# Kernel optimization log

Measured on AMD Instinct MI355X. Metric: run time of the kernel, lower is better.

## Reference

```python
import jax, jax.numpy as jnp
import numpy as np

_GROUP_SIZES = [4096, 2048, 1024, 8192, 512, 3072, 6144, 1024]
_K = 2048
_N = 2048


def setup_inputs() -> dict:
    key = jax.random.key(0)
    keys = jax.random.split(key, len(_GROUP_SIZES) + 1)
    inp = {}
    for i, m in enumerate(_GROUP_SIZES):
        inp[f"A{i}"] = jax.random.normal(keys[i], (m, _K), dtype=jnp.float32)
    inp["B_shared"] = jax.random.normal(keys[-1], (_K, _N), dtype=jnp.float32)
    return inp


def reference(A0, A1, A2, A3, A4, A5, A6, A7, B_shared):
    # torch: cat([a @ B for a in group_A], dim=0)
    # Concatenating ragged groups first and doing one GEMM is the same math
    # (row-block structure of matmul), expressed as a single fused contraction.
    A_cat = jnp.concatenate([A0, A1, A2, A3, A4, A5, A6, A7], axis=0)  # [M_total, K]
    return A_cat @ B_shared  # [M_total, N]
```

## Files before the change

kernel.cpp:

```cpp
#include <hip/hip_runtime.h>
#include <hip/hip_bf16.h>

using short8  = __attribute__((ext_vector_type(8))) short;
using ushort8 = __attribute__((ext_vector_type(8))) unsigned short;
using f32x4   = __attribute__((ext_vector_type(4))) float;

#define GLB(p)  ((const __attribute__((address_space(1))) void*)(p))
#define LDSP(p) ((__attribute__((address_space(3))) void*)(p))

static __device__ __forceinline__ unsigned short f2bf(float f) {
    union { float f; unsigned u; } v; v.f = f;
    unsigned u = v.u;
    u += 0x7fffu + ((u >> 16) & 1u);
    return (unsigned short)(u >> 16);
}

#define K_DIM 2048
#define N_DIM 2048
#define M_TOTAL 26112
#define N_GROUPS 8

__global__ __launch_bounds__(256) void cvt_a_all(
        const float* __restrict__ A0, const float* __restrict__ A1,
        const float* __restrict__ A2, const float* __restrict__ A3,
        const float* __restrict__ A4, const float* __restrict__ A5,
        const float* __restrict__ A6, const float* __restrict__ A7,
        unsigned short* __restrict__ Acat) {
    int b = blockIdx.x;
    const float* src; int gb;
    if      (b < 256)  { src = A0; gb = 0;    }
    else if (b < 384)  { src = A1; gb = 256;  }
    else if (b < 448)  { src = A2; gb = 384;  }
    else if (b < 960)  { src = A3; gb = 448;  }
    else if (b < 992)  { src = A4; gb = 960;  }
    else if (b < 1184) { src = A5; gb = 992;  }
    else if (b < 1568) { src = A6; gb = 1184; }
    else               { src = A7; gb = 1568; }
    const float* s   = src  + (long)(b - gb) * 16 * K_DIM;
    unsigned short* d = Acat + (long)b * 16 * K_DIM;
    int t = threadIdx.x;
#pragma unroll 4
    for (int i = 0; i < 16; ++i) {
        long off = (long)i * K_DIM + t * 8;
        float4 x = *(const float4*)(s + off);
        float4 y = *(const float4*)(s + off + 4);
        ushort8 o;
        o[0] = f2bf(x.x); o[1] = f2bf(x.y); o[2] = f2bf(x.z); o[3] = f2bf(x.w);
        o[4] = f2bf(y.x); o[5] = f2bf(y.y); o[6] = f2bf(y.z); o[7] = f2bf(y.w);
        *(ushort8*)(d + off) = o;
    }
}

__global__ __launch_bounds__(256) void cvt_bt_kernel(const float* __restrict__ B,
                                                     unsigned short* __restrict__ Bt) {
    __shared__ float t[32][33];
    int bx = blockIdx.x, by = blockIdx.y;
    int tx = threadIdx.x, ty = threadIdx.y;
#pragma unroll
    for (int i = 0; i < 32; i += 8)
        t[ty + i][tx] = B[(long)(by * 32 + ty + i) * N_DIM + bx * 32 + tx];
    __syncthreads();
#pragma unroll
    for (int i = 0; i < 32; i += 8)
        Bt[(long)(bx * 32 + ty + i) * K_DIM + by * 32 + tx] = f2bf(t[tx][ty + i]);
}


#define PBAR() __builtin_amdgcn_s_barrier()
#define LGKM0() asm volatile("s_waitcnt lgkmcnt(0)" ::: "memory")
#define VMC(n)  asm volatile("s_waitcnt vmcnt(" #n ")" ::: "memory")

#define ST_A(BUF, H, L, TT)                                                        \
    __builtin_amdgcn_global_load_lds(                                              \
        GLB(aSt + (long)((H) * 128 + (L) * 64) * K_DIM + (TT) * 64),               \
        LDSP(lds + (BUF) * 32768 + (H) * 8192 + (L) * 4096 + w * 512), 16, 0, 0)
#define ST_B(BUF, H, L, TT)                                                        \
    __builtin_amdgcn_global_load_lds(                                              \
        GLB(bSt + (long)((H) * 128 + (L) * 64) * K_DIM + (TT) * 64),               \
        LDSP(lds + (BUF) * 32768 + 16384 + (H) * 8192 + (L) * 4096 + w * 512), 16, 0, 0)

#define MMQ(MH, NH, AV, BV)                                                        \
    _Pragma("unroll") for (int i = 0; i < 4; ++i)                                  \
    _Pragma("unroll") for (int j = 0; j < 2; ++j)                                  \
        acc[(MH) * 4 + i][(NH) * 2 + j] = __builtin_amdgcn_mfma_f32_16x16x32_bf16( \
            AV[i], BV[j], acc[(MH) * 4 + i][(NH) * 2 + j], 0, 0, 0);

#define TILE(BUF, T, DO1, DO2)                                                          \
    do {                                                                                \
        const unsigned short* pA = lds + (BUF) * 32768 + wm * 1024 + r16 * 64;          \
        const unsigned short* pB = lds + (BUF) * 32768 + 16384 + wn * 1024 + r16 * 64;  \
        short8 a0[4], a1[4], b00[2], b01[2], b10[2], b11[2];                            \
                                \
        _Pragma("unroll") for (int i = 0; i < 4; ++i) {                                 \
            a0[i] = *(const short8*)(pA + i * 2048 + c0 * 8);                           \
            a1[i] = *(const short8*)(pA + i * 2048 + c1 * 8);                           \
        }                                                                               \
        _Pragma("unroll") for (int j = 0; j < 2; ++j) {                                 \
            b00[j] = *(const short8*)(pB + j * 4096 + c0 * 8);                          \
            b01[j] = *(const short8*)(pB + j * 4096 + c1 * 8);                          \
        }                                                                               \
        if (DO1) { ST_A((BUF) ^ 1, 1, 0, (T) + 1); ST_A((BUF) ^ 1, 1, 1, (T) + 1); }    \
        PBAR(); LGKM0();                                                                \
        __builtin_amdgcn_s_setprio(1); MMQ(0, 0, a0, b00); MMQ(0, 0, a1, b01);          \
        __builtin_amdgcn_s_setprio(0); PBAR();                                          \
                          \
        _Pragma("unroll") for (int j = 0; j < 2; ++j) {                                 \
            b10[j] = *(const short8*)(pB + 8192 + j * 4096 + c0 * 8);                   \
            b11[j] = *(const short8*)(pB + 8192 + j * 4096 + c1 * 8);                   \
        }                                                                               \
        if (DO2) { ST_A((BUF), 0, 0, (T) + 2); ST_A((BUF), 0, 1, (T) + 2); }            \
        PBAR(); LGKM0();                                                                \
        __builtin_amdgcn_s_setprio(1); MMQ(0, 1, a0, b10); MMQ(0, 1, a1, b11);          \
        __builtin_amdgcn_s_setprio(0); PBAR();                                          \
                          \
        _Pragma("unroll") for (int i = 0; i < 4; ++i) {                                 \
            a0[i] = *(const short8*)(pA + 8192 + i * 2048 + c0 * 8);                    \
            a1[i] = *(const short8*)(pA + 8192 + i * 2048 + c1 * 8);                    \
        }                                                                               \
        if (DO2) { ST_B((BUF), 0, 0, (T) + 2); ST_B((BUF), 0, 1, (T) + 2); }            \
        PBAR(); LGKM0();                                                                \
        __builtin_amdgcn_s_setprio(1); MMQ(1, 0, a0, b00); MMQ(1, 0, a1, b01);          \
        __builtin_amdgcn_s_setprio(0); PBAR();                                          \
                                                        \
        if (DO2) { ST_B((BUF), 1, 0, (T) + 2); ST_B((BUF), 1, 1, (T) + 2); }            \
        __builtin_amdgcn_s_setprio(1); MMQ(1, 1, a0, b10); MMQ(1, 1, a1, b11);          \
        __builtin_amdgcn_s_setprio(0);                                                  \
    } while (0)

__global__ __launch_bounds__(512, 2) void gemm8_kernel(const unsigned short* __restrict__ Acat,
                                                       const unsigned short* __restrict__ Bt,
                                                       float* __restrict__ C) {
    __shared__ unsigned short lds[65536];

    int wg  = blockIdx.x;
    int swz = (wg & 7) * 102 + (wg >> 3);
    int mt  = swz >> 3, nt = swz & 7;
    int m0  = mt * 256, n0 = nt * 256;

    int tid = threadIdx.x;
    int l   = tid & 63;
    int w   = tid >> 6;
    int wm  = w >> 2;
    int wn  = w & 3;
    int r16 = l & 15, kc = l >> 4, x = l & 7;
    int c0  = kc ^ x;
    int c1  = (4 + kc) ^ x;

    int srow = tid >> 3;
    int sq   = (tid & 7) ^ (srow & 7);
    const unsigned short* aSt = Acat + (long)(m0 + srow) * K_DIM + sq * 8;
    const unsigned short* bSt = Bt   + (long)(n0 + srow) * K_DIM + sq * 8;

    f32x4 acc[8][4] = {};

    ST_A(0, 0, 0, 0); ST_A(0, 0, 1, 0); ST_A(0, 1, 0, 0); ST_A(0, 1, 1, 0);
    ST_B(0, 0, 0, 0); ST_B(0, 0, 1, 0); ST_B(0, 1, 0, 0); ST_B(0, 1, 1, 0);
    ST_A(1, 0, 0, 1); ST_A(1, 0, 1, 1);
    ST_B(1, 0, 0, 1); ST_B(1, 0, 1, 1); ST_B(1, 1, 0, 1); ST_B(1, 1, 1, 1);
    VMC(6); PBAR();

#pragma unroll 1
    for (int t = 0; t < 30; t += 2) {
        TILE(0, t, 1, 1);     VMC(6); PBAR();
        TILE(1, t + 1, 1, 1); VMC(6); PBAR();
    }
    TILE(0, 30, 1, 0); VMC(0); PBAR();
    TILE(1, 31, 0, 0);

    int orow = m0 + wm * 16 + (l >> 4) * 4;
    int ocol = n0 + wn * 16 + (l & 15);
#pragma unroll
    for (int i = 0; i < 8; ++i)
#pragma unroll
        for (int j = 0; j < 4; ++j)
#pragma unroll
            for (int q = 0; q < 4; ++q)
                C[(long)(orow + i * 32 + q) * N_DIM + (ocol + j * 64)] = acc[i][j][q];
}

__global__ void naive_gemm_kernel(const float* __restrict__ A, const float* __restrict__ B,
                                  float* __restrict__ C, int M) {
    __shared__ float As[16][16];
    __shared__ float Bs[16][17];
    int tx = threadIdx.x, ty = threadIdx.y;
    int row = blockIdx.y * 16 + ty;
    int col = blockIdx.x * 16 + tx;
    float s = 0.f;
    for (int k0 = 0; k0 < K_DIM; k0 += 16) {
        As[ty][tx] = A[(long)row * K_DIM + k0 + tx];
        Bs[ty][tx] = B[(long)(k0 + ty) * N_DIM + col];
        __syncthreads();
#pragma unroll
        for (int t = 0; t < 16; ++t) s += As[ty][t] * Bs[t][tx];
        __syncthreads();
    }
    C[(long)row * N_DIM + col] = s;
}

extern "C" void kernel_launch(void* const* d_in, const int* in_sizes, int n_in,
                              void* d_out, int out_size, void* d_ws, size_t ws_size,
                              hipStream_t stream) {
    static const int g_m[N_GROUPS]   = {4096, 2048, 1024, 8192, 512, 3072, 6144, 1024};
    static const int g_off[N_GROUPS] = {0, 4096, 6144, 7168, 15360, 15872, 18944, 25088};

    float* C = (float*)d_out;
    const size_t need = ((size_t)M_TOTAL * K_DIM + (size_t)N_DIM * K_DIM) * 2;

    if (ws_size >= need) {
        unsigned short* Acat = (unsigned short*)d_ws;
        unsigned short* Bt   = Acat + (size_t)M_TOTAL * K_DIM;

        cvt_a_all<<<M_TOTAL / 16, 256, 0, stream>>>(
            (const float*)d_in[0], (const float*)d_in[1], (const float*)d_in[2],
            (const float*)d_in[3], (const float*)d_in[4], (const float*)d_in[5],
            (const float*)d_in[6], (const float*)d_in[7], Acat);
        cvt_bt_kernel<<<dim3(N_DIM / 32, K_DIM / 32), dim3(32, 8), 0, stream>>>(
            (const float*)d_in[8], Bt);

        gemm8_kernel<<<(M_TOTAL / 256) * (N_DIM / 256), 512, 0, stream>>>(Acat, Bt, C);
    } else {
        for (int g = 0; g < N_GROUPS; ++g)
            naive_gemm_kernel<<<dim3(N_DIM / 16, g_m[g] / 16), dim3(16, 16), 0, stream>>>(
                (const float*)d_in[g], (const float*)d_in[8], C + (size_t)g_off[g] * N_DIM,
                g_m[g]);
    }
}
```

Measured before the change: 296.4 us.

## Switch GEMM to 32x32x16 MFMA tiles and fuse A/B conversion kernels

The GEMM inner tile moves from 16x16x32 to 32x32x16 bf16 MFMA instructions, with each wave owning 32x32 sub-blocks. This cuts LDS fragment loads per MFMA and the instruction count. The explicit lgkmcnt(0) waits are removed so the compiler schedules LDS waits itself. The separate A-conversion and B-transpose kernels are merged into one launch, with 64 blocks each serially transposing a full column strip of B, which saves a launch but may create a long tail.

```diff
diff --git a/kernel.cpp b/kernel.cpp
--- a/kernel.cpp
+++ b/kernel.cpp
@@ -4,6 +4,7 @@
 using short8  = __attribute__((ext_vector_type(8))) short;
 using ushort8 = __attribute__((ext_vector_type(8))) unsigned short;
 using f32x4   = __attribute__((ext_vector_type(4))) float;
+using f32x16  = __attribute__((ext_vector_type(16))) float;
 
 #define GLB(p)  ((const __attribute__((address_space(1))) void*)(p))
 #define LDSP(p) ((__attribute__((address_space(3))) void*)(p))
@@ -20,54 +21,56 @@
 #define M_TOTAL 26112
 #define N_GROUPS 8
 
-__global__ __launch_bounds__(256) void cvt_a_all(
+__global__ __launch_bounds__(256) void cvt_all(
         const float* __restrict__ A0, const float* __restrict__ A1,
         const float* __restrict__ A2, const float* __restrict__ A3,
         const float* __restrict__ A4, const float* __restrict__ A5,
         const float* __restrict__ A6, const float* __restrict__ A7,
-        unsigned short* __restrict__ Acat) {
-    int b = blockIdx.x;
-    const float* src; int gb;
-    if      (b < 256)  { src = A0; gb = 0;    }
-    else if (b < 384)  { src = A1; gb = 256;  }
-    else if (b < 448)  { src = A2; gb = 384;  }
-    else if (b < 960)  { src = A3; gb = 448;  }
-    else if (b < 992)  { src = A4; gb = 960;  }
-    else if (b < 1184) { src = A5; gb = 992;  }
-    else if (b < 1568) { src = A6; gb = 1184; }
-    else               { src = A7; gb = 1568; }
-    const float* s   = src  + (long)(b - gb) * 16 * K_DIM;
-    unsigned short* d = Acat + (long)b * 16 * K_DIM;
-    int t = threadIdx.x;
+        const float* __restrict__ B,
+        unsigned short* __restrict__ Acat, unsigned short* __restrict__ Bt) {
+    int b   = blockIdx.x;
+    int tid = threadIdx.x;
+    if (b < 64) {
+        __shared__ float t[32][33];
+        int tx = tid & 31, ty = tid >> 5;
+        for (int by = 0; by < 64; ++by) {
+#pragma unroll
+            for (int i = 0; i < 32; i += 8)
+                t[ty + i][tx] = B[(long)(by * 32 + ty + i) * N_DIM + b * 32 + tx];
+            __syncthreads();
+#pragma unroll
+            for (int i = 0; i < 32; i += 8)
+                Bt[(long)(b * 32 + ty + i) * K_DIM + by * 32 + tx] = f2bf(t[tx][ty + i]);
+            __syncthreads();
+        }
+    } else {
+        int ab = b - 64;
+        const float* src; int gb;
+        if      (ab < 256)  { src = A0; gb = 0;    }
+        else if (ab < 384)  { src = A1; gb = 256;  }
+        else if (ab < 448)  { src = A2; gb = 384;  }
+        else if (ab < 960)  { src = A3; gb = 448;  }
+        else if (ab < 992)  { src = A4; gb = 960;  }
+        else if (ab < 1184) { src = A5; gb = 992;  }
+        else if (ab < 1568) { src = A6; gb = 1184; }
+        else                { src = A7; gb = 1568; }
+        const float* s    = src  + (long)(ab - gb) * 16 * K_DIM;
+        unsigned short* d = Acat + (long)ab * 16 * K_DIM;
 #pragma unroll 4
-    for (int i = 0; i < 16; ++i) {
-        long off = (long)i * K_DIM + t * 8;
-        float4 x = *(const float4*)(s + off);
-        float4 y = *(const float4*)(s + off + 4);
-        ushort8 o;
-        o[0] = f2bf(x.x); o[1] = f2bf(x.y); o[2] = f2bf(x.z); o[3] = f2bf(x.w);
-        o[4] = f2bf(y.x); o[5] = f2bf(y.y); o[6] = f2bf(y.z); o[7] = f2bf(y.w);
-        *(ushort8*)(d + off) = o;
-    }
-}
-
-__global__ __launch_bounds__(256) void cvt_bt_kernel(const float* __restrict__ B,
-                                                     unsigned short* __restrict__ Bt) {
-    __shared__ float t[32][33];
-    int bx = blockIdx.x, by = blockIdx.y;
-    int tx = threadIdx.x, ty = threadIdx.y;
-#pragma unroll
-    for (int i = 0; i < 32; i += 8)
-        t[ty + i][tx] = B[(long)(by * 32 + ty + i) * N_DIM + bx * 32 + tx];
-    __syncthreads();
-#pragma unroll
-    for (int i = 0; i < 32; i += 8)
-        Bt[(long)(bx * 32 + ty + i) * K_DIM + by * 32 + tx] = f2bf(t[tx][ty + i]);
+        for (int i = 0; i < 16; ++i) {
+            long off = (long)i * K_DIM + tid * 8;
+            float4 x = *(const float4*)(s + off);
+            float4 y = *(const float4*)(s + off + 4);
+            ushort8 o;
+            o[0] = f2bf(x.x); o[1] = f2bf(x.y); o[2] = f2bf(x.z); o[3] = f2bf(x.w);
+            o[4] = f2bf(y.x); o[5] = f2bf(y.y); o[6] = f2bf(y.z); o[7] = f2bf(y.w);
+            *(ushort8*)(d + off) = o;
+        }
+    }
 }
 
 
 #define PBAR() __builtin_amdgcn_s_barrier()
-#define LGKM0() asm volatile("s_waitcnt lgkmcnt(0)" ::: "memory")
 #define VMC(n)  asm volatile("s_waitcnt vmcnt(" #n ")" ::: "memory")
 
 #define ST_A(BUF, H, L, TT)                                                        \
@@ -79,51 +82,58 @@
         GLB(bSt + (long)((H) * 128 + (L) * 64) * K_DIM + (TT) * 64),               \
         LDSP(lds + (BUF) * 32768 + 16384 + (H) * 8192 + (L) * 4096 + w * 512), 16, 0, 0)
 
-#define MMQ(MH, NH, AV, BV)                                                        \
-    _Pragma("unroll") for (int i = 0; i < 4; ++i)                                  \
-    _Pragma("unroll") for (int j = 0; j < 2; ++j)                                  \
-        acc[(MH) * 4 + i][(NH) * 2 + j] = __builtin_amdgcn_mfma_f32_16x16x32_bf16( \
-            AV[i], BV[j], acc[(MH) * 4 + i][(NH) * 2 + j], 0, 0, 0);
+#define MFMA32(A, B, Cacc) __builtin_amdgcn_mfma_f32_32x32x16_bf16((A), (B), (Cacc), 0, 0, 0)
 
 #define TILE(BUF, T, DO1, DO2)                                                          \
     do {                                                                                \
-        const unsigned short* pA = lds + (BUF) * 32768 + wm * 1024 + r16 * 64;          \
-        const unsigned short* pB = lds + (BUF) * 32768 + 16384 + wn * 1024 + r16 * 64;  \
-        short8 a0[4], a1[4], b00[2], b01[2], b10[2], b11[2];                            \
+        const unsigned short* pA = lds + (BUF) * 32768 + (wm * 32 + r32) * 64;          \
+        const unsigned short* pB = lds + (BUF) * 32768 + 16384 + (wn * 32 + r32) * 64;  \
+        short8 a0[4], a1[4], b0[4], b1[4];                                              \
                                 \
-        _Pragma("unroll") for (int i = 0; i < 4; ++i) {                                 \
-            a0[i] = *(const short8*)(pA + i * 2048 + c0 * 8);                           \
-            a1[i] = *(const short8*)(pA + i * 2048 + c1 * 8);                           \
-        }                                                                               \
-        _Pragma("unroll") for (int j = 0; j < 2; ++j) {                                 \
-            b00[j] = *(const short8*)(pB + j * 4096 + c0 * 8);                          \
-            b01[j] = *(const short8*)(pB + j * 4096 + c1 * 8);                          \
+        _Pragma("unroll") for (int s = 0; s < 4; ++s) {                                 \
+            a0[s] = *(const short8*)(pA + cs[s] * 8);                                   \
+            a1[s] = *(const short8*)(pA + 64 * 64 + cs[s] * 8);                         \
+            b0[s] = *(const short8*)(pB + cs[s] * 8);                                   \
         }                                                                               \
         if (DO1) { ST_A((BUF) ^ 1, 1, 0, (T) + 1); ST_A((BUF) ^ 1, 1, 1, (T) + 1); }    \
-        PBAR(); LGKM0();                                                                \
-        __builtin_amdgcn_s_setprio(1); MMQ(0, 0, a0, b00); MMQ(0, 0, a1, b01);          \
+        PBAR();                                                                         \
+        __builtin_amdgcn_s_setprio(1);                                                  \
+        _Pragma("unroll") for (int s = 0; s < 4; ++s) {                                 \
+            acc[0][0] = MFMA32(a0[s], b0[s], acc[0][0]);                                \
+            acc[1][0] = MFMA32(a1[s], b0[s], acc[1][0]);                                \
+        }                                                                               \
         __builtin_amdgcn_s_setprio(0); PBAR();                                          \
-                          \
-        _Pragma("unroll") for (int j = 0; j < 2; ++j) {                                 \
-            b10[j] = *(const short8*)(pB + 8192 + j * 4096 + c0 * 8);                   \
-            b11[j] = *(const short8*)(pB + 8192 + j * 4096 + c1 * 8);                   \
-        }                                                                               \
+                             \
+        _Pragma("unroll") for (int s = 0; s < 4; ++s)                                   \
+            b1[s] = *(const short8*)(pB + 128 * 64 + cs[s] * 8);                        \
         if (DO2) { ST_A((BUF), 0, 0, (T) + 2); ST_A((BUF), 0, 1, (T) + 2); }            \
-        PBAR(); LGKM0();                                                                \
-        __builtin_amdgcn_s_setprio(1); MMQ(0, 1, a0, b10); MMQ(0, 1, a1, b11);          \
+        PBAR();                                                                         \
+        __builtin_amdgcn_s_setprio(1);                                                  \
+        _Pragma("unroll") for (int s = 0; s < 4; ++s) {                                 \
+            acc[0][1] = MFMA32(a0[s], b1[s], acc[0][1]);                                \
+            acc[1][1] = MFMA32(a1[s], b1[s], acc[1][1]);                                \
+        }                                                                               \
         __builtin_amdgcn_s_setprio(0); PBAR();                                          \
-                          \
-        _Pragma("unroll") for (int i = 0; i < 4; ++i) {                                 \
-            a0[i] = *(const short8*)(pA + 8192 + i * 2048 + c0 * 8);                    \
-            a1[i] = *(const short8*)(pA + 8192 + i * 2048 + c1 * 8);                    \
+                           \
+        _Pragma("unroll") for (int s = 0; s < 4; ++s) {                                 \
+            a0[s] = *(const short8*)(pA + 128 * 64 + cs[s] * 8);                        \
+            a1[s] = *(const short8*)(pA + 192 * 64 + cs[s] * 8);                        \
         }                                                                               \
         if (DO2) { ST_B((BUF), 0, 0, (T) + 2); ST_B((BUF), 0, 1, (T) + 2); }            \
-        PBAR(); LGKM0();                                                                \
-        __builtin_amdgcn_s_setprio(1); MMQ(1, 0, a0, b00); MMQ(1, 0, a1, b01);          \
+        PBAR();                                                                         \
+        __builtin_amdgcn_s_setprio(1);                                                  \
+        _Pragma("unroll") for (int s = 0; s < 4; ++s) {                                 \
+            acc[2][0] = MFMA32(a0[s], b0[s], acc[2][0]);                                \
+            acc[3][0] = MFMA32(a1[s], b0[s], acc[3][0]);                                \
+        }                                                                               \
         __builtin_amdgcn_s_setprio(0); PBAR();                                          \
-                                                        \
+                              \
         if (DO2) { ST_B((BUF), 1, 0, (T) + 2); ST_B((BUF), 1, 1, (T) + 2); }            \
-        __builtin_amdgcn_s_setprio(1); MMQ(1, 1, a0, b10); MMQ(1, 1, a1, b11);          \
+        __builtin_amdgcn_s_setprio(1);                                                  \
+        _Pragma("unroll") for (int s = 0; s < 4; ++s) {                                 \
+            acc[2][1] = MFMA32(a0[s], b1[s], acc[2][1]);                                \
+            acc[3][1] = MFMA32(a1[s], b1[s], acc[3][1]);                                \
+        }                                                                               \
         __builtin_amdgcn_s_setprio(0);                                                  \
     } while (0)
 
@@ -142,16 +152,17 @@
     int w   = tid >> 6;
     int wm  = w >> 2;
     int wn  = w & 3;
-    int r16 = l & 15, kc = l >> 4, x = l & 7;
-    int c0  = kc ^ x;
-    int c1  = (4 + kc) ^ x;
+    int r32 = l & 31;
+    int hi  = l >> 5;
+    int e   = l & 7;
+    int cs[4] = { (0 + hi) ^ e, (2 + hi) ^ e, (4 + hi) ^ e, (6 + hi) ^ e };
 
     int srow = tid >> 3;
     int sq   = (tid & 7) ^ (srow & 7);
     const unsigned short* aSt = Acat + (long)(m0 + srow) * K_DIM + sq * 8;
     const unsigned short* bSt = Bt   + (long)(n0 + srow) * K_DIM + sq * 8;
 
-    f32x4 acc[8][4] = {};
+    f32x16 acc[4][2] = {};
 
     ST_A(0, 0, 0, 0); ST_A(0, 0, 1, 0); ST_A(0, 1, 0, 0); ST_A(0, 1, 1, 0);
     ST_B(0, 0, 0, 0); ST_B(0, 0, 1, 0); ST_B(0, 1, 0, 0); ST_B(0, 1, 1, 0);
@@ -167,15 +178,16 @@
     TILE(0, 30, 1, 0); VMC(0); PBAR();
     TILE(1, 31, 0, 0);
 
-    int orow = m0 + wm * 16 + (l >> 4) * 4;
-    int ocol = n0 + wn * 16 + (l & 15);
-#pragma unroll
-    for (int i = 0; i < 8; ++i)
-#pragma unroll
-        for (int j = 0; j < 4; ++j)
-#pragma unroll
-            for (int q = 0; q < 4; ++q)
-                C[(long)(orow + i * 32 + q) * N_DIM + (ocol + j * 64)] = acc[i][j][q];
+    int orow = m0 + wm * 32 + 4 * hi;
+    int ocol = n0 + wn * 32 + r32;
+#pragma unroll
+    for (int i = 0; i < 4; ++i)
+#pragma unroll
+        for (int j = 0; j < 2; ++j)
+#pragma unroll
+            for (int q = 0; q < 16; ++q)
+                C[(long)(orow + i * 64 + (q & 3) + 8 * (q >> 2)) * N_DIM +
+                  (ocol + j * 128)] = acc[i][j][q];
 }
 
 __global__ void naive_gemm_kernel(const float* __restrict__ A, const float* __restrict__ B,
@@ -210,12 +222,11 @@
         unsigned short* Acat = (unsigned short*)d_ws;
         unsigned short* Bt   = Acat + (size_t)M_TOTAL * K_DIM;
 
-        cvt_a_all<<<M_TOTAL / 16, 256, 0, stream>>>(
+        cvt_all<<<64 + M_TOTAL / 16, 256, 0, stream>>>(
             (const float*)d_in[0], (const float*)d_in[1], (const float*)d_in[2],
             (const float*)d_in[3], (const float*)d_in[4], (const float*)d_in[5],
-            (const float*)d_in[6], (const float*)d_in[7], Acat);
-        cvt_bt_kernel<<<dim3(N_DIM / 32, K_DIM / 32), dim3(32, 8), 0, stream>>>(
-            (const float*)d_in[8], Bt);
+            (const float*)d_in[6], (const float*)d_in[7], (const float*)d_in[8],
+            Acat, Bt);
 
         gemm8_kernel<<<(M_TOTAL / 256) * (N_DIM / 256), 512, 0, stream>>>(Acat, Bt, C);
     } else {
```

Result: slower. 357.8 us (+20.7%).

## Split tail-wave GEMM tiles into 128-row halves and drop explicit LDS waits

Applied to the files above, without the earlier changes.

The 816 tiles of 256x256 are now split so the first 768 keep the 256x256 path and the last 48 tiles each become two 128x256 workgroups using a new TILE128 pipeline. This targets the partial last wave on the CUs by spreading the tail across more workgroups. Separately, the explicit s_waitcnt lgkmcnt(0) after each barrier is removed, leaving the compiler to insert the LDS-read waits. That could change scheduling, and it risks reading registers before the LDS loads finish if the compiler's waits are not placed correctly.

```diff
diff --git a/kernel.cpp b/kernel.cpp
--- a/kernel.cpp
+++ b/kernel.cpp
@@ -36,7 +36,7 @@
     else if (b < 1184) { src = A5; gb = 992;  }
     else if (b < 1568) { src = A6; gb = 1184; }
     else               { src = A7; gb = 1568; }
-    const float* s   = src  + (long)(b - gb) * 16 * K_DIM;
+    const float* s    = src  + (long)(b - gb) * 16 * K_DIM;
     unsigned short* d = Acat + (long)b * 16 * K_DIM;
     int t = threadIdx.x;
 #pragma unroll 4
@@ -67,7 +67,6 @@
 
 
 #define PBAR() __builtin_amdgcn_s_barrier()
-#define LGKM0() asm volatile("s_waitcnt lgkmcnt(0)" ::: "memory")
 #define VMC(n)  asm volatile("s_waitcnt vmcnt(" #n ")" ::: "memory")
 
 #define ST_A(BUF, H, L, TT)                                                        \
@@ -90,7 +89,7 @@
         const unsigned short* pA = lds + (BUF) * 32768 + wm * 1024 + r16 * 64;          \
         const unsigned short* pB = lds + (BUF) * 32768 + 16384 + wn * 1024 + r16 * 64;  \
         short8 a0[4], a1[4], b00[2], b01[2], b10[2], b11[2];                            \
-                                \
+                        \
         _Pragma("unroll") for (int i = 0; i < 4; ++i) {                                 \
             a0[i] = *(const short8*)(pA + i * 2048 + c0 * 8);                           \
             a1[i] = *(const short8*)(pA + i * 2048 + c1 * 8);                           \
@@ -100,82 +99,175 @@
             b01[j] = *(const short8*)(pB + j * 4096 + c1 * 8);                          \
         }                                                                               \
         if (DO1) { ST_A((BUF) ^ 1, 1, 0, (T) + 1); ST_A((BUF) ^ 1, 1, 1, (T) + 1); }    \
-        PBAR(); LGKM0();                                                                \
+        PBAR();                                                                         \
         __builtin_amdgcn_s_setprio(1); MMQ(0, 0, a0, b00); MMQ(0, 0, a1, b01);          \
         __builtin_amdgcn_s_setprio(0); PBAR();                                          \
-                          \
+                                 \
         _Pragma("unroll") for (int j = 0; j < 2; ++j) {                                 \
             b10[j] = *(const short8*)(pB + 8192 + j * 4096 + c0 * 8);                   \
             b11[j] = *(const short8*)(pB + 8192 + j * 4096 + c1 * 8);                   \
         }                                                                               \
         if (DO2) { ST_A((BUF), 0, 0, (T) + 2); ST_A((BUF), 0, 1, (T) + 2); }            \
-        PBAR(); LGKM0();                                                                \
+        PBAR();                                                                         \
         __builtin_amdgcn_s_setprio(1); MMQ(0, 1, a0, b10); MMQ(0, 1, a1, b11);          \
         __builtin_amdgcn_s_setprio(0); PBAR();                                          \
-                          \
+                                 \
         _Pragma("unroll") for (int i = 0; i < 4; ++i) {                                 \
             a0[i] = *(const short8*)(pA + 8192 + i * 2048 + c0 * 8);                    \
             a1[i] = *(const short8*)(pA + 8192 + i * 2048 + c1 * 8);                    \
         }                                                                               \
         if (DO2) { ST_B((BUF), 0, 0, (T) + 2); ST_B((BUF), 0, 1, (T) + 2); }            \
-        PBAR(); LGKM0();                                                                \
+        PBAR();                                                                         \
         __builtin_amdgcn_s_setprio(1); MMQ(1, 0, a0, b00); MMQ(1, 0, a1, b01);          \
         __builtin_amdgcn_s_setprio(0); PBAR();                                          \
-                                                        \
+                             \
         if (DO2) { ST_B((BUF), 1, 0, (T) + 2); ST_B((BUF), 1, 1, (T) + 2); }            \
         __builtin_amdgcn_s_setprio(1); MMQ(1, 1, a0, b10); MMQ(1, 1, a1, b11);          \
         __builtin_amdgcn_s_setprio(0);                                                  \
     } while (0)
 
+#define ST_A1(BUF, L, TT)                                                          \
+    __builtin_amdgcn_global_load_lds(                                              \
+        GLB(aSt + (long)((L) * 64) * K_DIM + (TT) * 64),                           \
+        LDSP(lds + (BUF) * 8192 + (L) * 4096 + w * 512), 16, 0, 0)
+#define ST_B1(BUF, H, L, TT)                                                       \
+    __builtin_amdgcn_global_load_lds(                                              \
+        GLB(bSt + (long)((H) * 128 + (L) * 64) * K_DIM + (TT) * 64),               \
+        LDSP(lds + 16384 + (BUF) * 16384 + (H) * 8192 + (L) * 4096 + w * 512), 16, 0, 0)
+
+#define MMQ1(MH, NH, AV, BV)                                                       \
+    _Pragma("unroll") for (int i = 0; i < 2; ++i)                                  \
+    _Pragma("unroll") for (int j = 0; j < 2; ++j)                                  \
+        acc[(MH) * 2 + i][(NH) * 2 + j] = __builtin_amdgcn_mfma_f32_16x16x32_bf16( \
+            AV[i], BV[j], acc[(MH) * 2 + i][(NH) * 2 + j], 0, 0, 0);
+
+#define TILE128(BUF, T, DO2)                                                            \
+    do {                                                                                \
+        const unsigned short* pA = lds + (BUF) * 8192 + wm * 1024 + r16 * 64;           \
+        const unsigned short* pB = lds + 16384 + (BUF) * 16384 + wn * 1024 + r16 * 64;  \
+        short8 a0[2], a1[2], b00[2], b01[2], b10[2], b11[2];                            \
+                                                     \
+        _Pragma("unroll") for (int i = 0; i < 2; ++i) {                                 \
+            a0[i] = *(const short8*)(pA + i * 2048 + c0 * 8);                           \
+            a1[i] = *(const short8*)(pA + i * 2048 + c1 * 8);                           \
+        }                                                                               \
+        _Pragma("unroll") for (int j = 0; j < 2; ++j) {                                 \
+            b00[j] = *(const short8*)(pB + j * 4096 + c0 * 8);                          \
+            b01[j] = *(const short8*)(pB + j * 4096 + c1 * 8);                          \
+        }                                                                               \
+        PBAR();                                                                         \
+        __builtin_amdgcn_s_setprio(1); MMQ1(0, 0, a0, b00); MMQ1(0, 0, a1, b01);        \
+        __builtin_amdgcn_s_setprio(0); PBAR();                                          \
+                                                             \
+        _Pragma("unroll") for (int j = 0; j < 2; ++j) {                                 \
+            b10[j] = *(const short8*)(pB + 8192 + j * 4096 + c0 * 8);                   \
+            b11[j] = *(const short8*)(pB + 8192 + j * 4096 + c1 * 8);                   \
+        }                                                                               \
+        PBAR();                                                                         \
+        __builtin_amdgcn_s_setprio(1); MMQ1(0, 1, a0, b10); MMQ1(0, 1, a1, b11);        \
+        __builtin_amdgcn_s_setprio(0); PBAR();                                          \
+                                            \
+        _Pragma("unroll") for (int i = 0; i < 2; ++i) {                                 \
+            a0[i] = *(const short8*)(pA + 4096 + i * 2048 + c0 * 8);                    \
+            a1[i] = *(const short8*)(pA + 4096 + i * 2048 + c1 * 8);                    \
+        }                                                                               \
+        if (DO2) { ST_B1((BUF), 0, 0, (T) + 2); ST_B1((BUF), 0, 1, (T) + 2); }          \
+        PBAR();                                                                         \
+        __builtin_amdgcn_s_setprio(1); MMQ1(1, 0, a0, b00); MMQ1(1, 0, a1, b01);        \
+        __builtin_amdgcn_s_setprio(0); PBAR();                                          \
+                               \
+        if (DO2) { ST_B1((BUF), 1, 0, (T) + 2); ST_B1((BUF), 1, 1, (T) + 2);            \
+                   ST_A1((BUF), 0, (T) + 2);    ST_A1((BUF), 1, (T) + 2); }             \
+        __builtin_amdgcn_s_setprio(1); MMQ1(1, 1, a0, b10); MMQ1(1, 1, a1, b11);        \
+        __builtin_amdgcn_s_setprio(0);                                                  \
+    } while (0)
+
 __global__ __launch_bounds__(512, 2) void gemm8_kernel(const unsigned short* __restrict__ Acat,
                                                        const unsigned short* __restrict__ Bt,
                                                        float* __restrict__ C) {
     __shared__ unsigned short lds[65536];
 
     int wg  = blockIdx.x;
-    int swz = (wg & 7) * 102 + (wg >> 3);
-    int mt  = swz >> 3, nt = swz & 7;
-    int m0  = mt * 256, n0 = nt * 256;
-
     int tid = threadIdx.x;
     int l   = tid & 63;
     int w   = tid >> 6;
     int wm  = w >> 2;
     int wn  = w & 3;
-    int r16 = l & 15, kc = l >> 4, x = l & 7;
-    int c0  = kc ^ x;
-    int c1  = (4 + kc) ^ x;
-
+    int r16 = l & 15, kq = l >> 4, x = l & 7;
+    int c0  = kq ^ x;
+    int c1  = (4 + kq) ^ x;
     int srow = tid >> 3;
     int sq   = (tid & 7) ^ (srow & 7);
-    const unsigned short* aSt = Acat + (long)(m0 + srow) * K_DIM + sq * 8;
-    const unsigned short* bSt = Bt   + (long)(n0 + srow) * K_DIM + sq * 8;
-
-    f32x4 acc[8][4] = {};
-
-    ST_A(0, 0, 0, 0); ST_A(0, 0, 1, 0); ST_A(0, 1, 0, 0); ST_A(0, 1, 1, 0);
-    ST_B(0, 0, 0, 0); ST_B(0, 0, 1, 0); ST_B(0, 1, 0, 0); ST_B(0, 1, 1, 0);
-    ST_A(1, 0, 0, 1); ST_A(1, 0, 1, 1);
-    ST_B(1, 0, 0, 1); ST_B(1, 0, 1, 1); ST_B(1, 1, 0, 1); ST_B(1, 1, 1, 1);
-    VMC(6); PBAR();
+
+    if (wg < 768) {
+        int swz = (wg & 7) * 102 + (wg >> 3);
+        int mt  = swz >> 3, nt = swz & 7;
+        int m0  = mt * 256, n0 = nt * 256;
+
+        const unsigned short* aSt = Acat + (long)(m0 + srow) * K_DIM + sq * 8;
+        const unsigned short* bSt = Bt   + (long)(n0 + srow) * K_DIM + sq * 8;
+
+        f32x4 acc[8][4] = {};
+
+        ST_A(0, 0, 0, 0); ST_A(0, 0, 1, 0); ST_A(0, 1, 0, 0); ST_A(0, 1, 1, 0);
+        ST_B(0, 0, 0, 0); ST_B(0, 0, 1, 0); ST_B(0, 1, 0, 0); ST_B(0, 1, 1, 0);
+        ST_A(1, 0, 0, 1); ST_A(1, 0, 1, 1);
+        ST_B(1, 0, 0, 1); ST_B(1, 0, 1, 1); ST_B(1, 1, 0, 1); ST_B(1, 1, 1, 1);
+        VMC(6); PBAR();
 
 #pragma unroll 1
-    for (int t = 0; t < 30; t += 2) {
-        TILE(0, t, 1, 1);     VMC(6); PBAR();
-        TILE(1, t + 1, 1, 1); VMC(6); PBAR();
+        for (int t = 0; t < 30; t += 2) {
+            TILE(0, t, 1, 1);     VMC(6); PBAR();
+            TILE(1, t + 1, 1, 1); VMC(6); PBAR();
+        }
+        TILE(0, 30, 1, 0); VMC(0); PBAR();
+        TILE(1, 31, 0, 0);
+
+        int orow = m0 + wm * 16 + (l >> 4) * 4;
+        int ocol = n0 + wn * 16 + (l & 15);
+#pragma unroll
+        for (int i = 0; i < 8; ++i)
+#pragma unroll
+            for (int j = 0; j < 4; ++j)
+#pragma unroll
+                for (int q = 0; q < 4; ++q)
+                    C[(long)(orow + i * 32 + q) * N_DIM + (ocol + j * 64)] = acc[i][j][q];
+    } else {
+        int k    = wg - 768;
+        int o    = 768 + (k >> 1);
+        int half = k & 1;
+        int swz  = (o & 7) * 102 + (o >> 3);
+        int mt   = swz >> 3, nt = swz & 7;
+        int m0   = mt * 256 + half * 128, n0 = nt * 256;
+
+        const unsigned short* aSt = Acat + (long)(m0 + srow) * K_DIM + sq * 8;
+        const unsigned short* bSt = Bt   + (long)(n0 + srow) * K_DIM + sq * 8;
+
+        f32x4 acc[4][4] = {};
+
+        ST_A1(0, 0, 0); ST_A1(0, 1, 0);
+        ST_B1(0, 0, 0, 0); ST_B1(0, 0, 1, 0); ST_B1(0, 1, 0, 0); ST_B1(0, 1, 1, 0);
+        ST_A1(1, 0, 1); ST_A1(1, 1, 1);
+        ST_B1(1, 0, 0, 1); ST_B1(1, 0, 1, 1); ST_B1(1, 1, 0, 1); ST_B1(1, 1, 1, 1);
+        VMC(6); PBAR();
+
+#pragma unroll 1
+        for (int t = 0; t < 30; ++t) {
+            TILE128(t & 1, t, 1); VMC(6); PBAR();
+        }
+        TILE128(0, 30, 0); VMC(0); PBAR();
+        TILE128(1, 31, 0);
+
+        int orow = m0 + wm * 16 + (l >> 4) * 4;
+        int ocol = n0 + wn * 16 + (l & 15);
+#pragma unroll
+        for (int i = 0; i < 4; ++i)
+#pragma unroll
+            for (int j = 0; j < 4; ++j)
+#pragma unroll
+                for (int q = 0; q < 4; ++q)
+                    C[(long)(orow + i * 32 + q) * N_DIM + (ocol + j * 64)] = acc[i][j][q];
     }
-    TILE(0, 30, 1, 0); VMC(0); PBAR();
-    TILE(1, 31, 0, 0);
-
-    int orow = m0 + wm * 16 + (l >> 4) * 4;
-    int ocol = n0 + wn * 16 + (l & 15);
-#pragma unroll
-    for (int i = 0; i < 8; ++i)
-#pragma unroll
-        for (int j = 0; j < 4; ++j)
-#pragma unroll
-            for (int q = 0; q < 4; ++q)
-                C[(long)(orow + i * 32 + q) * N_DIM + (ocol + j * 64)] = acc[i][j][q];
 }
 
 __global__ void naive_gemm_kernel(const float* __restrict__ A, const float* __restrict__ B,
@@ -217,7 +309,7 @@
         cvt_bt_kernel<<<dim3(N_DIM / 32, K_DIM / 32), dim3(32, 8), 0, stream>>>(
             (const float*)d_in[8], Bt);
 
-        gemm8_kernel<<<(M_TOTAL / 256) * (N_DIM / 256), 512, 0, stream>>>(Acat, Bt, C);
+        gemm8_kernel<<<768 + 96, 512, 0, stream>>>(Acat, Bt, C);
     } else {
         for (int g = 0; g < N_GROUPS; ++g)
             naive_gemm_kernel<<<dim3(N_DIM / 16, g_m[g] / 16), dim3(16, 16), 0, stream>>>(
```

New measurement: 282.0 us. 1.05x faster.
